# Kernel tuning notes

Measured on AMD Instinct MI355X. Metric: run time of the kernel, lower is better.

The kernel has to match this reference:

```python
import math
import jax, jax.numpy as jnp
import numpy as np

B = 65536
EMBED = 256
COND = 256
TIME = 128
HID = 256
E = 8
RHID = 128
IN_DIM = EMBED + TIME + COND  # 640


def setup_inputs() -> dict:
    key = jax.random.key(0)
    ks = jax.random.split(key, 20)
    s = 0.02
    inp = {
        "z_t": jax.random.normal(ks[0], (B, EMBED), jnp.float32),
        "t": jax.random.uniform(ks[1], (B, 1), jnp.float32),
        "cond": jax.random.normal(ks[2], (B, COND), jnp.float32),
        # time embedding proj (Linear(time,time) -> SiLU -> Linear(time,time))
        "tW1": jax.random.normal(ks[3], (TIME, TIME), jnp.float32) * s,
        "tb1": jnp.zeros((TIME,), jnp.float32),
        "tW2": jax.random.normal(ks[4], (TIME, TIME), jnp.float32) * s,
        "tb2": jnp.zeros((TIME,), jnp.float32),
        # stacked expert weights [E, in, out]
        "eW1": jax.random.normal(ks[5], (E, IN_DIM, HID), jnp.float32) * s,
        "eb1": jnp.zeros((E, HID), jnp.float32),
        "eW2": jax.random.normal(ks[6], (E, HID, HID), jnp.float32) * s,
        "eb2": jnp.zeros((E, HID), jnp.float32),
        "eW3": jax.random.normal(ks[7], (E, HID, EMBED), jnp.float32) * s,
        "eb3": jnp.zeros((E, EMBED), jnp.float32),
        # router
        "rW1": jax.random.normal(ks[8], (IN_DIM, RHID), jnp.float32) * s,
        "rb1": jnp.zeros((RHID,), jnp.float32),
        "rW2": jax.random.normal(ks[9], (RHID, E), jnp.float32) * s,
        "rb2": jnp.zeros((E,), jnp.float32),
    }
    return inp


def _time_embedding(t, tW1, tb1, tW2, tb2):
    half = TIME // 2  # 64
    scale = -math.log(10000.0) / (half - 1)
    freqs = jnp.exp(jnp.arange(half, dtype=t.dtype) * scale)[None, :]  # [1, half]
    angles = t * freqs  # [B, half]
    emb = jnp.concatenate([jnp.sin(angles), jnp.cos(angles)], axis=-1)  # [B, TIME]
    h = jax.nn.silu(emb @ tW1 + tb1)
    return h @ tW2 + tb2


def reference(z_t, t, cond, tW1, tb1, tW2, tb2, eW1, eb1, eW2, eb2, eW3, eb3, rW1, rb1, rW2, rb2):
    time_emb = _time_embedding(t, tW1, tb1, tW2, tb2)
    x = jnp.concatenate([z_t, time_emb, cond], axis=-1)  # [B, IN_DIM]
    # dense MoE: all experts via batched GEMMs (dropout=0 -> identity)
    h1 = jax.nn.silu(jnp.einsum('bi,eih->beh', x, eW1) + eb1)      # [B,E,HID]
    h2 = jax.nn.silu(jnp.einsum('beh,ehk->bek', h1, eW2) + eb2)    # [B,E,HID]
    expert_out = jnp.einsum('beh,ehd->bed', h2, eW3) + eb3         # [B,E,EMBED]
    # router softmax gate
    rh = jax.nn.silu(x @ rW1 + rb1)
    gate = jax.nn.softmax(rh @ rW2 + rb2, axis=-1)                 # [B,E]
    velocity = jnp.einsum('be,bed->bd', gate, expert_out)          # [B,EMBED]
    return velocity, gate
```

## Files before the change

### kernel.cpp

```cpp
#include <hip/hip_runtime.h>

typedef __attribute__((ext_vector_type(8))) short bf16x8;
typedef __attribute__((ext_vector_type(4))) float f32x4;

#define NB_ROWS 65536
#define D_EMBED 256
#define D_HID   256
#define N_EXP   8
#define D_RHID  128
#define D_IN    640
#define D_H1    2048

#define KSTR 72
#define HSTR 264

static __device__ __forceinline__ ushort f2bf(float f) {
  union { float f; unsigned u; } v; v.f = f;
  unsigned r = v.u + 0x7fffu + ((v.u >> 16) & 1u);
  return (ushort)(r >> 16);
}
static __device__ __forceinline__ float bf2f(ushort h) {
  union { unsigned u; float f; } v; v.u = ((unsigned)h) << 16;
  return v.f;
}
static __device__ __forceinline__ float silu_f(float x) {
  return x / (1.0f + __expf(-x));
}

static __device__ __forceinline__ int kswz(int r, int c) {
  return r * 64 + ((((c) >> 3) ^ (r & 7)) << 3) + ((c) & 7);
}

__global__ void prep_transpose(const float* __restrict__ src, ushort* __restrict__ dst,
                               int R, int C, int total) {
  int idx = blockIdx.x * 256 + threadIdx.x;
  if (idx >= total) return;
  int rc = R * C;
  int m = idx / rc;
  int rem = idx - m * rc;
  int r = rem / C;
  int c = rem - r * C;
  dst[m * rc + c * R + r] = f2bf(src[idx]);
}
__global__ void prep_transpose_swz(const float* __restrict__ src, ushort* __restrict__ dst,
                                   int R, int C, int total) {
  int idx = blockIdx.x * 256 + threadIdx.x;
  if (idx >= total) return;
  int rc = R * C;
  int m = idx / rc;
  int rem = idx - m * rc;
  int r = rem / C;
  int c = rem - r * C;
  int p = (r & ~63) + (((((r >> 3) & 7) ^ (c & 7)) << 3) | (r & 7));
  dst[m * rc + c * R + p] = f2bf(src[idx]);
}

static __device__ __forceinline__ void glB256_512(const ushort* __restrict__ src, int ld,
                                                  int kt, ushort* dst, int tid, int w) {
  #pragma unroll
  for (int c = 0; c < 4; ++c) {
    int f = c * 8192 + tid * 16;
    int r = f >> 7, ce = (f & 127) >> 1;
    __builtin_amdgcn_global_load_lds(
        (const __attribute__((address_space(1))) void*)(src + (size_t)r * ld + kt + ce),
        (__attribute__((address_space(3))) void*)(dst + ((c * 8192 + w * 1024) >> 1)),
        16, 0, 0);
  }
}
static __device__ __forceinline__ void stA128s(const ushort* __restrict__ src, int ld,
                                               int kt, ushort* dst, int tid) {
  uint4 v[2];
  #pragma unroll
  for (int c = 0; c < 2; ++c) {
    int f = c * 8192 + tid * 16;
    int r = f >> 7, ce = (f & 127) >> 1;
    v[c] = *(const uint4*)&src[(size_t)r * ld + kt + ce];
  }
  #pragma unroll
  for (int c = 0; c < 2; ++c) {
    int f = c * 8192 + tid * 16;
    int r = f >> 7, ce = (f & 127) >> 1;
    *(uint4*)&dst[kswz(r, ce)] = v[c];
  }
}
static __device__ __forceinline__ void stB256lin(const ushort* __restrict__ src, int ld,
                                                 int kt, ushort* dst, int tid) {
  uint4 v[4];
  #pragma unroll
  for (int c = 0; c < 4; ++c) {
    int f = c * 8192 + tid * 16;
    int r = f >> 7, ce = (f & 127) >> 1;
    v[c] = *(const uint4*)&src[(size_t)r * ld + kt + ce];
  }
  #pragma unroll
  for (int c = 0; c < 4; ++c) {
    int f = c * 8192 + tid * 16;
    int r = f >> 7, ce = (f & 127) >> 1;
    *(uint4*)&dst[r * 64 + ce] = v[c];
  }
}
static __device__ __forceinline__ void stageA128_256(const ushort* __restrict__ src, int ld,
                                                     int kt, ushort* dst, int tid) {
  uint4 v[4];
  #pragma unroll
  for (int c = 0; c < 4; ++c) {
    int f = c * 4096 + tid * 16;
    int r = f >> 7, ce = (f & 127) >> 1;
    v[c] = *(const uint4*)&src[(size_t)r * ld + kt + ce];
  }
  #pragma unroll
  for (int c = 0; c < 4; ++c) {
    int f = c * 4096 + tid * 16;
    int r = f >> 7, ce = (f & 127) >> 1;
    *(uint4*)&dst[r * KSTR + ce] = v[c];
  }
}

__global__ __launch_bounds__(512) void time_x_kernel(
    const float* __restrict__ zt, const float* __restrict__ tin,
    const float* __restrict__ cond,
    const ushort* __restrict__ tw1t, const ushort* __restrict__ tw2t,
    const float* __restrict__ tb1, const float* __restrict__ tb2,
    ushort* __restrict__ x) {
  __shared__ __align__(16) ushort sE[128 * 136];
  __shared__ float sFreq[64];
  __shared__ float sB1[128];
  __shared__ float sB2[128];

  const int tid = threadIdx.x;
  const int row0 = blockIdx.x * 128;

  for (int ch = tid; ch < 128 * 64; ch += 512) {
    int r = ch >> 6;
    int c4 = (ch & 63) << 2;
    size_t grow = (size_t)(row0 + r);
    float4 zv = *(const float4*)&zt[grow * 256 + c4];
    ushort4 o; o.x = f2bf(zv.x); o.y = f2bf(zv.y); o.z = f2bf(zv.z); o.w = f2bf(zv.w);
    *(ushort4*)&x[grow * 640 + c4] = o;
    float4 cv = *(const float4*)&cond[grow * 256 + c4];
    ushort4 o2; o2.x = f2bf(cv.x); o2.y = f2bf(cv.y); o2.z = f2bf(cv.z); o2.w = f2bf(cv.w);
    *(ushort4*)&x[grow * 640 + 384 + c4] = o2;
  }

  if (tid < 64) sFreq[tid] = __expf((float)tid * (-9.210340371976184f / 63.0f));
  if (tid < 128) { sB1[tid] = tb1[tid]; sB2[tid] = tb2[tid]; }
  __syncthreads();

  {
    int r = tid >> 2;
    int qd = tid & 3;
    float tv = tin[row0 + r];
    int half = qd >> 1;
    int cbase = (qd & 1) * 32;
    ushort* er = &sE[r * 136 + half * 64 + cbase];
    #pragma unroll
    for (int c = 0; c < 32; ++c) {
      float a = tv * sFreq[cbase + c];
      float v = half ? __cosf(a) : __sinf(a);
      er[c] = f2bf(v);
    }
  }
  __syncthreads();

  const int l = tid & 63;
  const int w = tid >> 6;
  const int wm = w >> 1;
  const int wn = w & 1;
  const int lr = l & 15;
  const int lk = (l >> 4) * 8;
  const int q4 = (l >> 4) * 4;

  f32x4 acc[2][4] = {};
  #pragma unroll
  for (int kk = 0; kk < 4; ++kk) {
    int kb = kk * 32 + lk;
    bf16x8 av[2], bv[4];
    #pragma unroll
    for (int mf = 0; mf < 2; ++mf)
      av[mf] = *(const bf16x8*)&sE[(wm * 32 + mf * 16 + lr) * 136 + kb];
    #pragma unroll
    for (int nf = 0; nf < 4; ++nf)
      bv[nf] = *(const bf16x8*)&tw1t[(size_t)(wn * 64 + nf * 16 + lr) * 128 + kb];
    #pragma unroll
    for (int mf = 0; mf < 2; ++mf)
      #pragma unroll
      for (int nf = 0; nf < 4; ++nf)
        acc[mf][nf] = __builtin_amdgcn_mfma_f32_16x16x32_bf16(av[mf], bv[nf], acc[mf][nf], 0, 0, 0);
  }
  __syncthreads();
  #pragma unroll
  for (int mf = 0; mf < 2; ++mf)
    #pragma unroll
    for (int nf = 0; nf < 4; ++nf) {
      int cc = wn * 64 + nf * 16 + lr;
      #pragma unroll
      for (int rg = 0; rg < 4; ++rg) {
        int rr = wm * 32 + mf * 16 + q4 + rg;
        sE[rr * 136 + cc] = f2bf(silu_f(acc[mf][nf][rg] + sB1[cc]));
      }
    }
  __syncthreads();

  f32x4 acc2[2][4] = {};
  #pragma unroll
  for (int kk = 0; kk < 4; ++kk) {
    int kb = kk * 32 + lk;
    bf16x8 av[2], bv[4];
    #pragma unroll
    for (int mf = 0; mf < 2; ++mf)
      av[mf] = *(const bf16x8*)&sE[(wm * 32 + mf * 16 + lr) * 136 + kb];
    #pragma unroll
    for (int nf = 0; nf < 4; ++nf)
      bv[nf] = *(const bf16x8*)&tw2t[(size_t)(wn * 64 + nf * 16 + lr) * 128 + kb];
    #pragma unroll
    for (int mf = 0; mf < 2; ++mf)
      #pragma unroll
      for (int nf = 0; nf < 4; ++nf)
        acc2[mf][nf] = __builtin_amdgcn_mfma_f32_16x16x32_bf16(av[mf], bv[nf], acc2[mf][nf], 0, 0, 0);
  }
  #pragma unroll
  for (int mf = 0; mf < 2; ++mf)
    #pragma unroll
    for (int nf = 0; nf < 4; ++nf) {
      int cc = wn * 64 + nf * 16 + lr;
      #pragma unroll
      for (int rg = 0; rg < 4; ++rg) {
        int rr = wm * 32 + mf * 16 + q4 + rg;
        x[(size_t)(row0 + rr) * 640 + 256 + cc] = f2bf(acc2[mf][nf][rg] + sB2[cc]);
      }
    }
}

__global__ __launch_bounds__(256) void router_kernel(
    const ushort* __restrict__ xb, const ushort* __restrict__ rw1t,
    const float* __restrict__ rb1, const float* __restrict__ rW2,
    const float* __restrict__ rb2, float* __restrict__ gatef,
    float* __restrict__ gateo) {
  __shared__ __align__(16) ushort smA[128 * KSTR];
  __shared__ __align__(16) ushort smB[128 * KSTR];
  __shared__ __align__(16) ushort rhbuf[128 * 136];
  __shared__ float sW2[128 * 8];

  const int tid = threadIdx.x;
  const int row0 = blockIdx.x * 128;
  for (int i = tid; i < 1024; i += 256) sW2[i] = rW2[i];

  const int l = tid & 63;
  const int w = tid >> 6;
  const int wm = w >> 1, wn = w & 1;
  const int lr = l & 15, lk = (l >> 4) * 8, q4 = (l >> 4) * 4;
  const ushort* xrow = xb + (size_t)row0 * 640;

  f32x4 acc[4][4] = {};
  for (int kt = 0; kt < 640; kt += 64) {
    stageA128_256(xrow, 640, kt, smA, tid);
    stageA128_256(rw1t, 640, kt, smB, tid);
    __syncthreads();
    #pragma unroll
    for (int kk = 0; kk < 2; ++kk) {
      int kb = kk * 32 + lk;
      bf16x8 av[4], bv[4];
      #pragma unroll
      for (int mf = 0; mf < 4; ++mf)
        av[mf] = *(const bf16x8*)&smA[(wm * 64 + mf * 16 + lr) * KSTR + kb];
      #pragma unroll
      for (int nf = 0; nf < 4; ++nf)
        bv[nf] = *(const bf16x8*)&smB[(wn * 64 + nf * 16 + lr) * KSTR + kb];
      #pragma unroll
      for (int mf = 0; mf < 4; ++mf)
        #pragma unroll
        for (int nf = 0; nf < 4; ++nf)
          acc[mf][nf] = __builtin_amdgcn_mfma_f32_16x16x32_bf16(av[mf], bv[nf], acc[mf][nf], 0, 0, 0);
    }
    __syncthreads();
  }
  #pragma unroll
  for (int nf = 0; nf < 4; ++nf) {
    int cc = wn * 64 + nf * 16 + lr;
    float b1v = rb1[cc];
    #pragma unroll
    for (int mf = 0; mf < 4; ++mf)
      #pragma unroll
      for (int rg = 0; rg < 4; ++rg) {
        int rr = wm * 64 + mf * 16 + q4 + rg;
        rhbuf[rr * 136 + cc] = f2bf(silu_f(acc[mf][nf][rg] + b1v));
      }
  }
  __syncthreads();

  if (tid < 128) {
    float a[8];
    #pragma unroll
    for (int e = 0; e < 8; ++e) a[e] = rb2[e];
    #pragma unroll
    for (int i8 = 0; i8 < 16; ++i8) {
      bf16x8 hv = *(const bf16x8*)&rhbuf[tid * 136 + i8 * 8];
      #pragma unroll
      for (int j = 0; j < 8; ++j) {
        float h = bf2f((ushort)hv[j]);
        const float* wrow = &sW2[(i8 * 8 + j) * 8];
        #pragma unroll
        for (int e = 0; e < 8; ++e) a[e] += h * wrow[e];
      }
    }
    float mx = a[0];
    #pragma unroll
    for (int e = 1; e < 8; ++e) mx = fmaxf(mx, a[e]);
    float s = 0.f, ex[8];
    #pragma unroll
    for (int e = 0; e < 8; ++e) { ex[e] = __expf(a[e] - mx); s += ex[e]; }
    float inv = 1.f / s;
    size_t b = (size_t)(row0 + tid);
    #pragma unroll
    for (int e = 0; e < 8; ++e) {
      float g = ex[e] * inv;
      gatef[b * 8 + e] = g;
      gateo[b * 8 + e] = g;
    }
  }
}

__global__ __launch_bounds__(512) void moe_h1_kernel(
    const ushort* __restrict__ xb, const ushort* __restrict__ w1t,
    const float* __restrict__ eb1, ushort* __restrict__ hg, int row_base) {
  __shared__ __align__(16) ushort smA[128 * 64];
  __shared__ __align__(16) ushort smB[256 * 64];

  const int tid = threadIdx.x;
  int nwg = gridDim.x;
  int flat = blockIdx.x;
  int sid = (flat & 7) * (nwg >> 3) + (flat >> 3);
  const int rb = sid >> 3;
  const int e  = sid & 7;
  const int lrow0 = rb * 128;

  const int l = tid & 63;
  const int w = tid >> 6;
  const int wm = w >> 2, wn = w & 3;
  const int lr = l & 15, lk = (l >> 4) * 8, q4 = (l >> 4) * 4;

  const ushort* xrow = xb + (size_t)(row_base + lrow0) * 640;
  const ushort* W1 = w1t + (size_t)e * (256 * 640);

  f32x4 acc[4][4] = {};
  for (int kt = 0; kt < 640; kt += 64) {
    stA128s(xrow, 640, kt, smA, tid);
    glB256_512(W1, 640, kt, smB, tid, w);
    __syncthreads();
    #pragma unroll
    for (int kk = 0; kk < 2; ++kk) {
      int kb = kk * 32 + lk;
      bf16x8 av[4], bv[4];
      #pragma unroll
      for (int mf = 0; mf < 4; ++mf)
        av[mf] = *(const bf16x8*)&smA[kswz(wm * 64 + mf * 16 + lr, kb)];
      #pragma unroll
      for (int nf = 0; nf < 4; ++nf)
        bv[nf] = *(const bf16x8*)&smB[kswz(wn * 64 + nf * 16 + lr, kb)];
      #pragma unroll
      for (int mf = 0; mf < 4; ++mf)
        #pragma unroll
        for (int nf = 0; nf < 4; ++nf)
          acc[mf][nf] = __builtin_amdgcn_mfma_f32_16x16x32_bf16(av[mf], bv[nf], acc[mf][nf], 0, 0, 0);
    }
    __syncthreads();
  }
  #pragma unroll
  for (int nf = 0; nf < 4; ++nf) {
    int cc = wn * 64 + nf * 16 + lr;
    float b1v = eb1[e * 256 + cc];
    #pragma unroll
    for (int mf = 0; mf < 4; ++mf)
      #pragma unroll
      for (int rg = 0; rg < 4; ++rg) {
        int rr = wm * 64 + mf * 16 + q4 + rg;
        hg[(size_t)(lrow0 + rr) * D_H1 + e * 256 + cc] = f2bf(silu_f(acc[mf][nf][rg] + b1v));
      }
  }
}

__global__ __launch_bounds__(512) void moe_h2_kernel(
    ushort* __restrict__ hg, const ushort* __restrict__ w2t,
    const float* __restrict__ eb2, const float* __restrict__ gatef, int row_base) {
  __shared__ __align__(16) ushort smA[128 * 64];
  __shared__ __align__(16) ushort smB[256 * 64];
  __shared__ float sGate[128];

  const int tid = threadIdx.x;
  int nwg = gridDim.x;
  int flat = blockIdx.x;
  int sid = (flat & 7) * (nwg >> 3) + (flat >> 3);
  const int rb = sid >> 3;
  const int e  = sid & 7;
  const int lrow0 = rb * 128;

  const int l = tid & 63;
  const int w = tid >> 6;
  const int wm = w >> 2, wn = w & 3;
  const int lr = l & 15, lk = (l >> 4) * 8, q4 = (l >> 4) * 4;

  if (tid < 128) sGate[tid] = gatef[(size_t)(row_base + lrow0 + tid) * 8 + e];

  ushort* hrow = hg + (size_t)lrow0 * D_H1 + e * 256;
  const ushort* W2 = w2t + (size_t)e * (256 * 256);

  f32x4 acc[4][4] = {};
  for (int kt = 0; kt < 256; kt += 64) {
    stA128s(hrow, D_H1, kt, smA, tid);
    glB256_512(W2, 256, kt, smB, tid, w);
    __syncthreads();
    #pragma unroll
    for (int kk = 0; kk < 2; ++kk) {
      int kb = kk * 32 + lk;
      bf16x8 av[4], bv[4];
      #pragma unroll
      for (int mf = 0; mf < 4; ++mf)
        av[mf] = *(const bf16x8*)&smA[kswz(wm * 64 + mf * 16 + lr, kb)];
      #pragma unroll
      for (int nf = 0; nf < 4; ++nf)
        bv[nf] = *(const bf16x8*)&smB[kswz(wn * 64 + nf * 16 + lr, kb)];
      #pragma unroll
      for (int mf = 0; mf < 4; ++mf)
        #pragma unroll
        for (int nf = 0; nf < 4; ++nf)
          acc[mf][nf] = __builtin_amdgcn_mfma_f32_16x16x32_bf16(av[mf], bv[nf], acc[mf][nf], 0, 0, 0);
    }
    __syncthreads();
  }
  #pragma unroll
  for (int nf = 0; nf < 4; ++nf) {
    int cc = wn * 64 + nf * 16 + lr;
    float b2v = eb2[e * 256 + cc];
    #pragma unroll
    for (int mf = 0; mf < 4; ++mf)
      #pragma unroll
      for (int rg = 0; rg < 4; ++rg) {
        int rr = wm * 64 + mf * 16 + q4 + rg;
        hrow[(size_t)rr * D_H1 + cc] = f2bf(silu_f(acc[mf][nf][rg] + b2v) * sGate[rr]);
      }
  }
}

__global__ __launch_bounds__(512) void moe_vel_kernel(
    const ushort* __restrict__ hg, const ushort* __restrict__ w3t,
    const float* __restrict__ eb3, const float* __restrict__ gatef,
    float* __restrict__ velout, int row_base) {
  __shared__ __align__(16) ushort smA[128 * 64];
  __shared__ __align__(16) ushort smB[256 * 64];
  __shared__ float sGate[128 * 8];

  const int tid = threadIdx.x;
  int nwg = gridDim.x;
  int flat = blockIdx.x;
  int sid = (flat & 7) * (nwg >> 3) + (flat >> 3);
  const int lrow0 = sid * 128;

  const int l = tid & 63;
  const int w = tid >> 6;
  const int wm = w >> 2, wn = w & 3;
  const int lr = l & 15, lk = (l >> 4) * 8, q4 = (l >> 4) * 4;

  for (int i = tid; i < 1024; i += 512) sGate[i] = gatef[(size_t)(row_base + lrow0) * 8 + i];

  const ushort* hrow = hg + (size_t)lrow0 * D_H1;
  f32x4 vacc[4][4] = {};
  __syncthreads();

  for (int kt = 0; kt < 2048; kt += 64) {
    const int e = kt >> 8;
    stA128s(hrow, D_H1, kt, smA, tid);
    glB256_512(w3t + (size_t)e * (256 * 256), 256, kt & 255, smB, tid, w);
    __syncthreads();
    #pragma unroll
    for (int kk = 0; kk < 2; ++kk) {
      int kb = kk * 32 + lk;
      bf16x8 av[4], bv[4];
      #pragma unroll
      for (int mf = 0; mf < 4; ++mf)
        av[mf] = *(const bf16x8*)&smA[kswz(wm * 64 + mf * 16 + lr, kb)];
      #pragma unroll
      for (int nf = 0; nf < 4; ++nf)
        bv[nf] = *(const bf16x8*)&smB[kswz(wn * 64 + nf * 16 + lr, kb)];
      #pragma unroll
      for (int mf = 0; mf < 4; ++mf)
        #pragma unroll
        for (int nf = 0; nf < 4; ++nf)
          vacc[mf][nf] = __builtin_amdgcn_mfma_f32_16x16x32_bf16(av[mf], bv[nf], vacc[mf][nf], 0, 0, 0);
    }
    __syncthreads();
  }

  float* eL = (float*)smB;
  for (int i = tid; i < 2048; i += 512) eL[i] = eb3[i];
  __syncthreads();
  #pragma unroll
  for (int mf = 0; mf < 4; ++mf)
    #pragma unroll
    for (int rg = 0; rg < 4; ++rg) {
      int rr = wm * 64 + mf * 16 + q4 + rg;
      const float* gp = &sGate[rr * 8];
      #pragma unroll
      for (int nf = 0; nf < 4; ++nf) {
        int cc = wn * 64 + nf * 16 + lr;
        float bsum = 0.f;
        #pragma unroll
        for (int ee = 0; ee < 8; ++ee) bsum += gp[ee] * eL[ee * 256 + cc];
        velout[(size_t)(row_base + lrow0 + rr) * D_EMBED + cc] = vacc[mf][nf][rg] + bsum;
      }
    }
}

__global__ __launch_bounds__(512) void moe_fused_kernel(
    const ushort* __restrict__ xb, const ushort* __restrict__ w1t,
    const ushort* __restrict__ w2t, const ushort* __restrict__ w3t,
    const float* __restrict__ eb1, const float* __restrict__ eb2,
    const float* __restrict__ eb3, const float* __restrict__ gatef,
    float* __restrict__ velout) {
  __shared__ __align__(16) ushort smA[128 * 64];
  __shared__ __align__(16) ushort smB[256 * 64];
  __shared__ __align__(16) ushort hbuf[128 * HSTR];
  __shared__ float sGate[128 * 8];
  __shared__ float sEb3[8 * 256];

  const int tid = threadIdx.x;
  const int row0 = blockIdx.x * 128;
  const int l = tid & 63;
  const int w = tid >> 6;
  const int wm = w >> 2, wn = w & 3;
  const int lr = l & 15, lk = (l >> 4) * 8, q4 = (l >> 4) * 4;

  for (int i = tid; i < 1024; i += 512) sGate[i] = gatef[(size_t)row0 * 8 + i];
  for (int i = tid; i < 2048; i += 512) sEb3[i] = eb3[i];

  const ushort* xrow = xb + (size_t)row0 * 640;
  f32x4 vacc[4][4] = {};
  __syncthreads();

  for (int e = 0; e < 8; ++e) {
    const ushort* W1 = w1t + (size_t)e * (256 * 640);
    const ushort* W2 = w2t + (size_t)e * (256 * 256);
    const ushort* W3 = w3t + (size_t)e * (256 * 256);

    f32x4 acc[4][4] = {};
    for (int kt = 0; kt < 640; kt += 64) {
      stA128s(xrow, 640, kt, smA, tid);
      stB256lin(W1, 640, kt, smB, tid);
      __syncthreads();
      #pragma unroll
      for (int kk = 0; kk < 2; ++kk) {
        int kb = kk * 32 + lk;
        bf16x8 av[4], bv[4];
        #pragma unroll
        for (int mf = 0; mf < 4; ++mf)
          av[mf] = *(const bf16x8*)&smA[kswz(wm * 64 + mf * 16 + lr, kb)];
        #pragma unroll
        for (int nf = 0; nf < 4; ++nf)
          bv[nf] = *(const bf16x8*)&smB[kswz(wn * 64 + nf * 16 + lr, kb)];
        #pragma unroll
        for (int mf = 0; mf < 4; ++mf)
          #pragma unroll
          for (int nf = 0; nf < 4; ++nf)
            acc[mf][nf] = __builtin_amdgcn_mfma_f32_16x16x32_bf16(av[mf], bv[nf], acc[mf][nf], 0, 0, 0);
      }
      __syncthreads();
    }
    #pragma unroll
    for (int nf = 0; nf < 4; ++nf) {
      int cc = wn * 64 + nf * 16 + lr;
      float b1v = eb1[e * 256 + cc];
      #pragma unroll
      for (int mf = 0; mf < 4; ++mf)
        #pragma unroll
        for (int rg = 0; rg < 4; ++rg) {
          int rr = wm * 64 + mf * 16 + q4 + rg;
          hbuf[rr * HSTR + cc] = f2bf(silu_f(acc[mf][nf][rg] + b1v));
        }
    }
    __syncthreads();

    #pragma unroll
    for (int mf = 0; mf < 4; ++mf)
      #pragma unroll
      for (int nf = 0; nf < 4; ++nf)
        acc[mf][nf] = (f32x4){0.f, 0.f, 0.f, 0.f};
    for (int kt = 0; kt < 256; kt += 64) {
      stB256lin(W2, 256, kt, smB, tid);
      __syncthreads();
      #pragma unroll
      for (int kk = 0; kk < 2; ++kk) {
        int kbl = kk * 32 + lk;
        int kbh = kt + kbl;
        bf16x8 av[4], bv[4];
        #pragma unroll
        for (int mf = 0; mf < 4; ++mf)
          av[mf] = *(const bf16x8*)&hbuf[(wm * 64 + mf * 16 + lr) * HSTR + kbh];
        #pragma unroll
        for (int nf = 0; nf < 4; ++nf)
          bv[nf] = *(const bf16x8*)&smB[kswz(wn * 64 + nf * 16 + lr, kbl)];
        #pragma unroll
        for (int mf = 0; mf < 4; ++mf)
          #pragma unroll
          for (int nf = 0; nf < 4; ++nf)
            acc[mf][nf] = __builtin_amdgcn_mfma_f32_16x16x32_bf16(av[mf], bv[nf], acc[mf][nf], 0, 0, 0);
      }
      __syncthreads();
    }
    #pragma unroll
    for (int nf = 0; nf < 4; ++nf) {
      int cc = wn * 64 + nf * 16 + lr;
      float b2v = eb2[e * 256 + cc];
      #pragma unroll
      for (int mf = 0; mf < 4; ++mf)
        #pragma unroll
        for (int rg = 0; rg < 4; ++rg) {
          int rr = wm * 64 + mf * 16 + q4 + rg;
          float gv = sGate[rr * 8 + e];
          hbuf[rr * HSTR + cc] = f2bf(silu_f(acc[mf][nf][rg] + b2v) * gv);
        }
    }
    __syncthreads();

    for (int kt = 0; kt < 256; kt += 64) {
      stB256lin(W3, 256, kt, smB, tid);
      __syncthreads();
      #pragma unroll
      for (int kk = 0; kk < 2; ++kk) {
        int kbl = kk * 32 + lk;
        int kbh = kt + kbl;
        bf16x8 av[4], bv[4];
        #pragma unroll
        for (int mf = 0; mf < 4; ++mf)
          av[mf] = *(const bf16x8*)&hbuf[(wm * 64 + mf * 16 + lr) * HSTR + kbh];
        #pragma unroll
        for (int nf = 0; nf < 4; ++nf)
          bv[nf] = *(const bf16x8*)&smB[kswz(wn * 64 + nf * 16 + lr, kbl)];
        #pragma unroll
        for (int mf = 0; mf < 4; ++mf)
          #pragma unroll
          for (int nf = 0; nf < 4; ++nf)
            vacc[mf][nf] = __builtin_amdgcn_mfma_f32_16x16x32_bf16(av[mf], bv[nf], vacc[mf][nf], 0, 0, 0);
      }
      __syncthreads();
    }
  }

  #pragma unroll
  for (int mf = 0; mf < 4; ++mf)
    #pragma unroll
    for (int rg = 0; rg < 4; ++rg) {
      int rr = wm * 64 + mf * 16 + q4 + rg;
      const float* gp = &sGate[rr * 8];
      #pragma unroll
      for (int nf = 0; nf < 4; ++nf) {
        int cc = wn * 64 + nf * 16 + lr;
        float bsum = 0.f;
        #pragma unroll
        for (int ee = 0; ee < 8; ++ee) bsum += gp[ee] * sEb3[ee * 256 + cc];
        velout[(size_t)(row0 + rr) * D_EMBED + cc] = vacc[mf][nf][rg] + bsum;
      }
    }
}

extern "C" void kernel_launch(void* const* d_in, const int* in_sizes, int n_in,
                              void* d_out, int out_size, void* d_ws, size_t ws_size,
                              hipStream_t stream) {
  const float* zt   = (const float*)d_in[0];
  const float* tin  = (const float*)d_in[1];
  const float* cond = (const float*)d_in[2];
  const float* tW1  = (const float*)d_in[3];
  const float* tb1  = (const float*)d_in[4];
  const float* tW2  = (const float*)d_in[5];
  const float* tb2  = (const float*)d_in[6];
  const float* eW1  = (const float*)d_in[7];
  const float* eb1  = (const float*)d_in[8];
  const float* eW2  = (const float*)d_in[9];
  const float* eb2  = (const float*)d_in[10];
  const float* eW3  = (const float*)d_in[11];
  const float* eb3  = (const float*)d_in[12];
  const float* rW1  = (const float*)d_in[13];
  const float* rb1  = (const float*)d_in[14];
  const float* rW2  = (const float*)d_in[15];
  const float* rb2  = (const float*)d_in[16];

  char* wp = (char*)d_ws;
  ushort* xb    = (ushort*)wp; wp += (size_t)NB_ROWS * D_IN * 2;
  float*  gatef = (float*)wp;  wp += (size_t)NB_ROWS * 8 * 4;
  ushort* w1t   = (ushort*)wp; wp += (size_t)N_EXP * D_HID * D_IN * 2;
  ushort* w2t   = (ushort*)wp; wp += (size_t)N_EXP * D_HID * D_HID * 2;
  ushort* w3t   = (ushort*)wp; wp += (size_t)N_EXP * D_HID * D_EMBED * 2;
  ushort* rw1t  = (ushort*)wp; wp += (size_t)D_RHID * D_IN * 2;
  ushort* tw1t  = (ushort*)wp; wp += (size_t)128 * 128 * 2;
  ushort* tw2t  = (ushort*)wp; wp += (size_t)128 * 128 * 2;
  ushort* hg    = (ushort*)wp;
  size_t base = (size_t)(wp - (char*)d_ws);

  int CH = 0;
  for (int cand = NB_ROWS; cand >= 8192; cand >>= 1) {
    if (base + (size_t)cand * D_H1 * 2 <= ws_size) { CH = cand; break; }
  }

  float* velout  = (float*)d_out;
  float* gateout = velout + (size_t)NB_ROWS * D_EMBED;

  {
    int tot;
    tot = 128 * 128;
    prep_transpose<<<(tot + 255) / 256, 256, 0, stream>>>(tW1, tw1t, 128, 128, tot);
    prep_transpose<<<(tot + 255) / 256, 256, 0, stream>>>(tW2, tw2t, 128, 128, tot);
    tot = D_IN * D_RHID;
    prep_transpose<<<(tot + 255) / 256, 256, 0, stream>>>(rW1, rw1t, D_IN, D_RHID, tot);
    tot = N_EXP * D_IN * D_HID;
    prep_transpose_swz<<<(tot + 255) / 256, 256, 0, stream>>>(eW1, w1t, D_IN, D_HID, tot);
    tot = N_EXP * D_HID * D_HID;
    prep_transpose_swz<<<(tot + 255) / 256, 256, 0, stream>>>(eW2, w2t, D_HID, D_HID, tot);
    tot = N_EXP * D_HID * D_EMBED;
    prep_transpose_swz<<<(tot + 255) / 256, 256, 0, stream>>>(eW3, w3t, D_HID, D_EMBED, tot);
  }

  time_x_kernel<<<512, 512, 0, stream>>>(zt, tin, cond, tw1t, tw2t, tb1, tb2, xb);
  router_kernel<<<512, 256, 0, stream>>>(xb, rw1t, rb1, rW2, rb2, gatef, gateout);

  if (CH > 0) {
    for (int r0 = 0; r0 < NB_ROWS; r0 += CH) {
      moe_h1_kernel<<<(CH / 128) * 8, 512, 0, stream>>>(xb, w1t, eb1, hg, r0);
      moe_h2_kernel<<<(CH / 128) * 8, 512, 0, stream>>>(hg, w2t, eb2, gatef, r0);
      moe_vel_kernel<<<CH / 128, 512, 0, stream>>>(hg, w3t, eb3, gatef, velout, r0);
    }
  } else {
    moe_fused_kernel<<<512, 512, 0, stream>>>(xb, w1t, w2t, w3t,
                                              eb1, eb2, eb3, gatef, velout);
  }
}
```

Baseline: 649.1 us.

## Pre-swizzle activations in global memory and stage A tiles via direct-to-LDS loads

Writes x, h1 and h2 in global memory in an XOR-swizzled column order, so A tiles can be copied straight into shared memory with global_load_lds instead of going through registers and a swizzled LDS store. The router also switches to swizzled LDS tiles fed by direct loads, and its weight prep now uses the swizzled transpose. This cuts register staging and VALU address work in every GEMM main loop. In exchange the global layout of intermediates becomes implicit, and every producer and consumer of those buffers must agree on the swizzle.

```diff
diff --git a/kernel.cpp b/kernel.cpp
--- a/kernel.cpp
+++ b/kernel.cpp
@@ -11,7 +11,6 @@
 #define D_IN    640
 #define D_H1    2048
 
-#define KSTR 72
 #define HSTR 264
 
 static __device__ __forceinline__ ushort f2bf(float f) {
@@ -29,6 +28,9 @@
 
 static __device__ __forceinline__ int kswz(int r, int c) {
   return r * 64 + ((((c) >> 3) ^ (r & 7)) << 3) + ((c) & 7);
+}
+static __device__ __forceinline__ int gswz(int r, int c) {
+  return ((c) & ~63) | (((((c) >> 3) & 7) ^ ((r) & 7)) << 3) | ((c) & 7);
 }
 
 __global__ void prep_transpose(const float* __restrict__ src, ushort* __restrict__ dst,
@@ -55,6 +57,18 @@
   dst[m * rc + c * R + p] = f2bf(src[idx]);
 }
 
+static __device__ __forceinline__ void glA128_512(const ushort* __restrict__ src, int ld,
+                                                  int kt, ushort* dst, int tid, int w) {
+  #pragma unroll
+  for (int c = 0; c < 2; ++c) {
+    int f = c * 8192 + tid * 16;
+    int r = f >> 7, ce = (f & 127) >> 1;
+    __builtin_amdgcn_global_load_lds(
+        (const __attribute__((address_space(1))) void*)(src + (size_t)r * ld + kt + ce),
+        (__attribute__((address_space(3))) void*)(dst + ((c * 8192 + w * 1024) >> 1)),
+        16, 0, 0);
+  }
+}
 static __device__ __forceinline__ void glB256_512(const ushort* __restrict__ src, int ld,
                                                   int kt, ushort* dst, int tid, int w) {
   #pragma unroll
@@ -67,52 +81,16 @@
         16, 0, 0);
   }
 }
-static __device__ __forceinline__ void stA128s(const ushort* __restrict__ src, int ld,
-                                               int kt, ushort* dst, int tid) {
-  uint4 v[2];
-  #pragma unroll
-  for (int c = 0; c < 2; ++c) {
-    int f = c * 8192 + tid * 16;
-    int r = f >> 7, ce = (f & 127) >> 1;
-    v[c] = *(const uint4*)&src[(size_t)r * ld + kt + ce];
-  }
-  #pragma unroll
-  for (int c = 0; c < 2; ++c) {
-    int f = c * 8192 + tid * 16;
-    int r = f >> 7, ce = (f & 127) >> 1;
-    *(uint4*)&dst[kswz(r, ce)] = v[c];
-  }
-}
-static __device__ __forceinline__ void stB256lin(const ushort* __restrict__ src, int ld,
-                                                 int kt, ushort* dst, int tid) {
-  uint4 v[4];
-  #pragma unroll
-  for (int c = 0; c < 4; ++c) {
-    int f = c * 8192 + tid * 16;
-    int r = f >> 7, ce = (f & 127) >> 1;
-    v[c] = *(const uint4*)&src[(size_t)r * ld + kt + ce];
-  }
-  #pragma unroll
-  for (int c = 0; c < 4; ++c) {
-    int f = c * 8192 + tid * 16;
-    int r = f >> 7, ce = (f & 127) >> 1;
-    *(uint4*)&dst[r * 64 + ce] = v[c];
-  }
-}
-static __device__ __forceinline__ void stageA128_256(const ushort* __restrict__ src, int ld,
-                                                     int kt, ushort* dst, int tid) {
-  uint4 v[4];
+static __device__ __forceinline__ void glB128_256(const ushort* __restrict__ src, int ld,
+                                                  int kt, ushort* dst, int tid, int w) {
   #pragma unroll
   for (int c = 0; c < 4; ++c) {
     int f = c * 4096 + tid * 16;
     int r = f >> 7, ce = (f & 127) >> 1;
-    v[c] = *(const uint4*)&src[(size_t)r * ld + kt + ce];
-  }
-  #pragma unroll
-  for (int c = 0; c < 4; ++c) {
-    int f = c * 4096 + tid * 16;
-    int r = f >> 7, ce = (f & 127) >> 1;
-    *(uint4*)&dst[r * KSTR + ce] = v[c];
+    __builtin_amdgcn_global_load_lds(
+        (const __attribute__((address_space(1))) void*)(src + (size_t)r * ld + kt + ce),
+        (__attribute__((address_space(3))) void*)(dst + ((c * 4096 + w * 1024) >> 1)),
+        16, 0, 0);
   }
 }
 
@@ -136,10 +114,10 @@
     size_t grow = (size_t)(row0 + r);
     float4 zv = *(const float4*)&zt[grow * 256 + c4];
     ushort4 o; o.x = f2bf(zv.x); o.y = f2bf(zv.y); o.z = f2bf(zv.z); o.w = f2bf(zv.w);
-    *(ushort4*)&x[grow * 640 + c4] = o;
+    *(ushort4*)&x[grow * 640 + gswz(r, c4)] = o;
     float4 cv = *(const float4*)&cond[grow * 256 + c4];
     ushort4 o2; o2.x = f2bf(cv.x); o2.y = f2bf(cv.y); o2.z = f2bf(cv.z); o2.w = f2bf(cv.w);
-    *(ushort4*)&x[grow * 640 + 384 + c4] = o2;
+    *(ushort4*)&x[grow * 640 + gswz(r, 384 + c4)] = o2;
   }
 
   if (tid < 64) sFreq[tid] = __expf((float)tid * (-9.210340371976184f / 63.0f));
@@ -226,7 +204,7 @@
       #pragma unroll
       for (int rg = 0; rg < 4; ++rg) {
         int rr = wm * 32 + mf * 16 + q4 + rg;
-        x[(size_t)(row0 + rr) * 640 + 256 + cc] = f2bf(acc2[mf][nf][rg] + sB2[cc]);
+        x[(size_t)(row0 + rr) * 640 + gswz(rr, 256 + cc)] = f2bf(acc2[mf][nf][rg] + sB2[cc]);
       }
     }
 }
@@ -236,8 +214,8 @@
     const float* __restrict__ rb1, const float* __restrict__ rW2,
     const float* __restrict__ rb2, float* __restrict__ gatef,
     float* __restrict__ gateo) {
-  __shared__ __align__(16) ushort smA[128 * KSTR];
-  __shared__ __align__(16) ushort smB[128 * KSTR];
+  __shared__ __align__(16) ushort smA[128 * 64];
+  __shared__ __align__(16) ushort smB[128 * 64];
   __shared__ __align__(16) ushort rhbuf[128 * 136];
   __shared__ float sW2[128 * 8];
 
@@ -253,8 +231,8 @@
 
   f32x4 acc[4][4] = {};
   for (int kt = 0; kt < 640; kt += 64) {
-    stageA128_256(xrow, 640, kt, smA, tid);
-    stageA128_256(rw1t, 640, kt, smB, tid);
+    glB128_256(xrow, 640, kt, smA, tid, w);
+    glB128_256(rw1t, 640, kt, smB, tid, w);
     __syncthreads();
     #pragma unroll
     for (int kk = 0; kk < 2; ++kk) {
@@ -262,10 +240,10 @@
       bf16x8 av[4], bv[4];
       #pragma unroll
       for (int mf = 0; mf < 4; ++mf)
-        av[mf] = *(const bf16x8*)&smA[(wm * 64 + mf * 16 + lr) * KSTR + kb];
+        av[mf] = *(const bf16x8*)&smA[kswz(wm * 64 + mf * 16 + lr, kb)];
       #pragma unroll
       for (int nf = 0; nf < 4; ++nf)
-        bv[nf] = *(const bf16x8*)&smB[(wn * 64 + nf * 16 + lr) * KSTR + kb];
+        bv[nf] = *(const bf16x8*)&smB[kswz(wn * 64 + nf * 16 + lr, kb)];
       #pragma unroll
       for (int mf = 0; mf < 4; ++mf)
         #pragma unroll
@@ -344,7 +322,7 @@
 
   f32x4 acc[4][4] = {};
   for (int kt = 0; kt < 640; kt += 64) {
-    stA128s(xrow, 640, kt, smA, tid);
+    glA128_512(xrow, 640, kt, smA, tid, w);
     glB256_512(W1, 640, kt, smB, tid, w);
     __syncthreads();
     #pragma unroll
@@ -374,7 +352,8 @@
       #pragma unroll
       for (int rg = 0; rg < 4; ++rg) {
         int rr = wm * 64 + mf * 16 + q4 + rg;
-        hg[(size_t)(lrow0 + rr) * D_H1 + e * 256 + cc] = f2bf(silu_f(acc[mf][nf][rg] + b1v));
+        hg[(size_t)(lrow0 + rr) * D_H1 + e * 256 + gswz(rr, cc)] =
+            f2bf(silu_f(acc[mf][nf][rg] + b1v));
       }
   }
 }
@@ -406,7 +385,7 @@
 
   f32x4 acc[4][4] = {};
   for (int kt = 0; kt < 256; kt += 64) {
-    stA128s(hrow, D_H1, kt, smA, tid);
+    glA128_512(hrow, D_H1, kt, smA, tid, w);
     glB256_512(W2, 256, kt, smB, tid, w);
     __syncthreads();
     #pragma unroll
@@ -436,7 +415,8 @@
       #pragma unroll
       for (int rg = 0; rg < 4; ++rg) {
         int rr = wm * 64 + mf * 16 + q4 + rg;
-        hrow[(size_t)rr * D_H1 + cc] = f2bf(silu_f(acc[mf][nf][rg] + b2v) * sGate[rr]);
+        hrow[(size_t)rr * D_H1 + gswz(rr, cc)] =
+            f2bf(silu_f(acc[mf][nf][rg] + b2v) * sGate[rr]);
       }
   }
 }
@@ -468,7 +448,7 @@
 
   for (int kt = 0; kt < 2048; kt += 64) {
     const int e = kt >> 8;
-    stA128s(hrow, D_H1, kt, smA, tid);
+    glA128_512(hrow, D_H1, kt, smA, tid, w);
     glB256_512(w3t + (size_t)e * (256 * 256), 256, kt & 255, smB, tid, w);
     __syncthreads();
     #pragma unroll
@@ -543,8 +523,8 @@
 
     f32x4 acc[4][4] = {};
     for (int kt = 0; kt < 640; kt += 64) {
-      stA128s(xrow, 640, kt, smA, tid);
-      stB256lin(W1, 640, kt, smB, tid);
+      glA128_512(xrow, 640, kt, smA, tid, w);
+      glB256_512(W1, 640, kt, smB, tid, w);
       __syncthreads();
       #pragma unroll
       for (int kk = 0; kk < 2; ++kk) {
@@ -584,7 +564,7 @@
       for (int nf = 0; nf < 4; ++nf)
         acc[mf][nf] = (f32x4){0.f, 0.f, 0.f, 0.f};
     for (int kt = 0; kt < 256; kt += 64) {
-      stB256lin(W2, 256, kt, smB, tid);
+      glB256_512(W2, 256, kt, smB, tid, w);
       __syncthreads();
       #pragma unroll
       for (int kk = 0; kk < 2; ++kk) {
@@ -621,7 +601,7 @@
     __syncthreads();
 
     for (int kt = 0; kt < 256; kt += 64) {
-      stB256lin(W3, 256, kt, smB, tid);
+      glB256_512(W3, 256, kt, smB, tid, w);
       __syncthreads();
       #pragma unroll
       for (int kk = 0; kk < 2; ++kk) {
@@ -708,7 +688,7 @@
     prep_transpose<<<(tot + 255) / 256, 256, 0, stream>>>(tW1, tw1t, 128, 128, tot);
     prep_transpose<<<(tot + 255) / 256, 256, 0, stream>>>(tW2, tw2t, 128, 128, tot);
     tot = D_IN * D_RHID;
-    prep_transpose<<<(tot + 255) / 256, 256, 0, stream>>>(rW1, rw1t, D_IN, D_RHID, tot);
+    prep_transpose_swz<<<(tot + 255) / 256, 256, 0, stream>>>(rW1, rw1t, D_IN, D_RHID, tot);
     tot = N_EXP * D_IN * D_HID;
     prep_transpose_swz<<<(tot + 255) / 256, 256, 0, stream>>>(eW1, w1t, D_IN, D_HID, tot);
     tot = N_EXP * D_HID * D_HID;
```

After: 656.6 us. No clear change (+1.1%).
